# Performance work log

Hardware: AMD Instinct MI355X
Metric: run time of the kernel (lower is better)

## Reference

```python
import jax, jax.numpy as jnp
import numpy as np

N_EMBD = 1024
N_HEAD = 16
HEAD_DIM = N_EMBD // N_HEAD
EPS = 1e-8


def rmsnorm(x, scale):
    return x * jax.lax.rsqrt(jnp.mean(x * x, axis=-1, keepdims=True) + EPS) * scale


def setup_inputs() -> dict:
    key = jax.random.key(0)
    ks = jax.random.split(key, 7)
    B, L, D = 4, 2048, N_EMBD
    s = lambda fan_in: 1.0 / np.sqrt(fan_in)
    return {
        "x": jax.random.normal(ks[0], (B, L, D), jnp.float32),
        "norm1_scale": jnp.ones((D,), jnp.float32),
        "w_qkv": jax.random.normal(ks[1], (D, 3 * D), jnp.float32) * s(D),
        "w_proj": jax.random.normal(ks[2], (D, D), jnp.float32) * s(D),
        "norm2_scale": jnp.ones((D,), jnp.float32),
        "w_fc1": jax.random.normal(ks[3], (D, 4 * D), jnp.float32) * s(D),
        "w_fc2": jax.random.normal(ks[4], (4 * D, D), jnp.float32) * s(4 * D),
    }


def reference(x, norm1_scale, w_qkv, w_proj, norm2_scale, w_fc1, w_fc2):
    B, L, D = x.shape
    H, hd = N_HEAD, HEAD_DIM

    # --- attention sub-block ---
    h = rmsnorm(x, norm1_scale)
    qkv = h @ w_qkv  # [B, L, 3D]
    q, k, v = jnp.split(qkv, 3, axis=-1)
    q = q.reshape(B, L, H, hd).transpose(0, 2, 1, 3)  # [B, H, L, hd]
    k = k.reshape(B, L, H, hd).transpose(0, 2, 1, 3)
    v = v.reshape(B, L, H, hd).transpose(0, 2, 1, 3)
    att = jnp.einsum("bhqd,bhkd->bhqk", q, k) * (hd ** -0.5)
    att = jax.nn.softmax(att, axis=-1)  # bidirectional, no mask
    out = jnp.einsum("bhqk,bhkd->bhqd", att, v)
    out = out.transpose(0, 2, 1, 3).reshape(B, L, D)
    x = x + out @ w_proj

    # --- MLP sub-block ---
    h = rmsnorm(x, norm2_scale)
    x = x + jax.nn.gelu(h @ w_fc1, approximate=False) @ w_fc2
    return x
```

## Files before the change

kernel.cpp:

```cpp
#include <hip/hip_runtime.h>
#include <hip/hip_bf16.h>
#include <cmath>


typedef __bf16 bf16x8 __attribute__((ext_vector_type(8)));
typedef __bf16 bf16x2 __attribute__((ext_vector_type(2)));
typedef float f32x4 __attribute__((ext_vector_type(4)));

__device__ __forceinline__ float bf2f(unsigned short u) {
  union { unsigned int i; float f; } c; c.i = ((unsigned int)u) << 16; return c.f;
}
__device__ __forceinline__ unsigned short f2bf(float f) {
  union { unsigned int i; float f; } c; c.f = f;
  unsigned int r = c.i + 0x7fffu + ((c.i >> 16) & 1u);
  return (unsigned short)(r >> 16);
}

__device__ __forceinline__ bool probe_bf16(const void* p) {
  return *reinterpret_cast<const unsigned int*>(p) == 0x3F803F80u;
}
__device__ __forceinline__ float ldext(const void* p, size_t i, bool isbf) {
  return isbf ? bf2f(reinterpret_cast<const unsigned short*>(p)[i])
              : reinterpret_cast<const float*>(p)[i];
}

__device__ __forceinline__ void cp16(const unsigned short* g, unsigned short* l) {
  __builtin_amdgcn_global_load_lds(
      (const __attribute__((address_space(1))) unsigned int*)g,
      (__attribute__((address_space(3))) unsigned int*)l,
      16, 0, 0);
}

__global__ __launch_bounds__(256) void transpose_any(
    const void* __restrict__ in, unsigned short* __restrict__ out,
    int R, int C, const void* __restrict__ probe) {
  const bool isbf = probe_bf16(probe);
  __shared__ unsigned short tile[32][33];
  const int bx = blockIdx.x * 32;
  const int by = blockIdx.y * 32;
  const int tx = threadIdx.x & 31, ty = threadIdx.x >> 5;
#pragma unroll
  for (int i = 0; i < 32; i += 8)
    tile[ty + i][tx] = f2bf(ldext(in, (size_t)(by + ty + i) * C + bx + tx, isbf));
  __syncthreads();
#pragma unroll
  for (int i = 0; i < 32; i += 8)
    out[(size_t)(bx + ty + i) * R + by + tx] = tile[tx][ty + i];
}

__device__ __forceinline__ void rmsnorm_body(
    const float v0, const float v1, const float v2, const float v3,
    const void* scale, bool isbf, unsigned short* outrow, int tid) {
  float ss = v0 * v0 + v1 * v1 + v2 * v2 + v3 * v3;
#pragma unroll
  for (int m = 32; m >= 1; m >>= 1) ss += __shfl_xor(ss, m);
  __shared__ float red[4];
  if ((tid & 63) == 0) red[tid >> 6] = ss;
  __syncthreads();
  ss = red[0] + red[1] + red[2] + red[3];
  const float rstd = rsqrtf(ss * (1.0f / 1024.0f) + 1e-8f);
  ushort4 o;
  o.x = f2bf(v0 * rstd * ldext(scale, tid * 4 + 0, isbf));
  o.y = f2bf(v1 * rstd * ldext(scale, tid * 4 + 1, isbf));
  o.z = f2bf(v2 * rstd * ldext(scale, tid * 4 + 2, isbf));
  o.w = f2bf(v3 * rstd * ldext(scale, tid * 4 + 3, isbf));
  reinterpret_cast<ushort4*>(outrow)[tid] = o;
}

__global__ __launch_bounds__(256) void rmsnorm_ext(
    const void* __restrict__ x, const void* __restrict__ scale,
    unsigned short* __restrict__ out, const void* __restrict__ probe) {
  const bool isbf = probe_bf16(probe);
  const int row = blockIdx.x, tid = threadIdx.x;
  float v0, v1, v2, v3;
  if (isbf) {
    ushort4 u = reinterpret_cast<const ushort4*>(x)[(size_t)row * 256 + tid];
    v0 = bf2f(u.x); v1 = bf2f(u.y); v2 = bf2f(u.z); v3 = bf2f(u.w);
  } else {
    float4 f = reinterpret_cast<const float4*>(x)[(size_t)row * 256 + tid];
    v0 = f.x; v1 = f.y; v2 = f.z; v3 = f.w;
  }
  rmsnorm_body(v0, v1, v2, v3, scale, isbf, out + (size_t)row * 1024, tid);
}

__global__ __launch_bounds__(256) void rmsnorm_int(
    const unsigned short* __restrict__ x, const void* __restrict__ scale,
    unsigned short* __restrict__ out, const void* __restrict__ probe) {
  const bool isbf = probe_bf16(probe);
  const int row = blockIdx.x, tid = threadIdx.x;
  ushort4 u = reinterpret_cast<const ushort4*>(x + (size_t)row * 1024)[tid];
  rmsnorm_body(bf2f(u.x), bf2f(u.y), bf2f(u.z), bf2f(u.w),
               scale, isbf, out + (size_t)row * 1024, tid);
}

template <int EPI, typename OutT>
__global__ __launch_bounds__(256) void gemm_bt(
    const unsigned short* __restrict__ A, const unsigned short* __restrict__ BT,
    OutT* __restrict__ C, const void* __restrict__ Res,
    int M, int N, int K, const void* __restrict__ probe) {
  __shared__ __align__(16) unsigned short As[128 * 64];
  __shared__ __align__(16) unsigned short Bs[128 * 64];
  const int tid = threadIdx.x;
  const int lane = tid & 63;
  const int w = tid >> 6;
  const int quad = lane >> 4;
  const int l16 = lane & 15;
  const int wr = w >> 1, wc = w & 1;
  const int m0 = blockIdx.y * 128;
  const int n0 = blockIdx.x * 128;

  const f32x4 zero = {0.f, 0.f, 0.f, 0.f};
  f32x4 acc[4][4];
#pragma unroll
  for (int i = 0; i < 4; ++i)
#pragma unroll
    for (int j = 0; j < 4; ++j) acc[i][j] = zero;

  for (int kt = 0; kt < K; kt += 64) {
#pragma unroll
    for (int i = 0; i < 4; ++i) {
      const int cb = (i * 4 + w) * 64;
      const int c = cb + lane;
      const int row = c >> 3;
      const int gc = (c & 7) ^ (row & 7);
      cp16(A + (size_t)(m0 + row) * K + kt + gc * 8, As + (size_t)cb * 8);
      cp16(BT + (size_t)(n0 + row) * K + kt + gc * 8, Bs + (size_t)cb * 8);
    }
    __syncthreads();

#pragma unroll
    for (int kk = 0; kk < 2; ++kk) {
      bf16x8 af[4], bfr[4];
#pragma unroll
      for (int mi = 0; mi < 4; ++mi)
        af[mi] = *reinterpret_cast<const bf16x8*>(
            As + (wr * 64 + mi * 16 + l16) * 64 + ((((kk << 2) + quad) ^ (l16 & 7)) << 3));
#pragma unroll
      for (int ni = 0; ni < 4; ++ni)
        bfr[ni] = *reinterpret_cast<const bf16x8*>(
            Bs + (wc * 64 + ni * 16 + l16) * 64 + ((((kk << 2) + quad) ^ (l16 & 7)) << 3));
#pragma unroll
      for (int mi = 0; mi < 4; ++mi)
#pragma unroll
        for (int ni = 0; ni < 4; ++ni)
          acc[mi][ni] = __builtin_amdgcn_mfma_f32_16x16x32_bf16(af[mi], bfr[ni], acc[mi][ni], 0, 0, 0);
    }
    __syncthreads();
  }

  if constexpr (EPI == 5) {
    if (n0 >= 2048) {
      unsigned short* vt = (unsigned short*)Res;
#pragma unroll
      for (int mi = 0; mi < 4; ++mi) {
        const int r0 = m0 + wr * 64 + mi * 16 + quad * 4;
        const int bq = r0 >> 11;
        const int key = r0 & 2047;
#pragma unroll
        for (int ni = 0; ni < 4; ++ni) {
          const int vcol = n0 - 2048 + wc * 64 + ni * 16 + l16;
          ushort4 o4;
          o4.x = f2bf(acc[mi][ni][0]); o4.y = f2bf(acc[mi][ni][1]);
          o4.z = f2bf(acc[mi][ni][2]); o4.w = f2bf(acc[mi][ni][3]);
          *reinterpret_cast<ushort4*>(
              vt + (((size_t)(bq * 1024 + vcol)) << 11) + key) = o4;
        }
      }
      return;
    }
  }

  const bool pb = (EPI == 3) ? probe_bf16(probe) : true;
#pragma unroll
  for (int mi = 0; mi < 4; ++mi) {
#pragma unroll
    for (int reg = 0; reg < 4; ++reg) {
      const int row = m0 + wr * 64 + mi * 16 + quad * 4 + reg;
#pragma unroll
      for (int ni = 0; ni < 4; ++ni) {
        const int col = n0 + wc * 64 + ni * 16 + l16;
        float v = acc[mi][ni][reg];
        if (EPI == 1) v = 0.5f * v * (1.0f + erff(v * 0.70710678118654752f));
        if (EPI == 2) v += bf2f(reinterpret_cast<const unsigned short*>(Res)[(size_t)row * N + col]);
        if (EPI == 3) v += ldext(Res, (size_t)row * N + col, pb);
        if ((EPI == 4 || EPI == 5) && col < 1024) v *= 0.18033688011112042f;
        if constexpr (sizeof(OutT) == 2)
          C[(size_t)row * N + col] = f2bf(v);
        else
          C[(size_t)row * N + col] = v;
      }
    }
  }
}

__global__ __launch_bounds__(256) void flash_attn(
    const unsigned short* __restrict__ qkv,
    const unsigned short* __restrict__ vT,
    unsigned short* __restrict__ out) {
  __shared__ __align__(16) unsigned short Ks[2][64 * 64];
  __shared__ __align__(16) unsigned short Vs[2][64 * 64];
  const int L = 2048, DQ = 3072, D = 1024;
  const int qt = blockIdx.x, h = blockIdx.y, b = blockIdx.z;
  const int tid = threadIdx.x, lane = tid & 63, w = tid >> 6;
  const int quad = lane >> 4, l16 = lane & 15;
  const int woff = w * 32;
  const unsigned short* base = qkv + (size_t)b * L * DQ;
  const unsigned short* vbase = vT + (size_t)(b * 1024 + h * 64) * 2048;

  unsigned short* Qs = &Vs[0][0];
#pragma unroll
  for (int i = 0; i < 4; ++i) {
    const int cb = i * 256 + w * 64;
    const int c = cb + lane;
    const int r = c >> 3, d8 = (c & 7) << 3;
    cp16(base + (size_t)(qt * 128 + r) * DQ + h * 64 + d8, Qs + ((size_t)cb << 3));
  }
  asm volatile("s_waitcnt vmcnt(0)" ::: "memory");
  __builtin_amdgcn_s_barrier();
  __builtin_amdgcn_sched_barrier(0);
  bf16x8 qf[2][2];
#pragma unroll
  for (int mj = 0; mj < 2; ++mj)
#pragma unroll
    for (int kc = 0; kc < 2; ++kc)
      qf[mj][kc] = *reinterpret_cast<const bf16x8*>(
          Qs + (woff + mj * 16 + l16) * 64 + kc * 32 + quad * 8);
  asm volatile("s_waitcnt lgkmcnt(0)" ::: "memory");
  __builtin_amdgcn_sched_barrier(0);
  __builtin_amdgcn_s_barrier();

  auto STAGE = [&](int s, int kt0) {
#pragma unroll
    for (int i = 0; i < 2; ++i) {
      const int cb = i * 256 + w * 64;
      const int cd = cb + lane;
      const int m = cd >> 3, cc = cd & 7;
      const int gk = ((m >> 4) & 1) * 32 + ((m >> 2) & 3) * 8 + (m >> 5) * 4 + (m & 3);
      const int gc = cc ^ (m & 7);
      cp16(base + (size_t)(kt0 + gk) * DQ + 1024 + h * 64 + gc * 8,
           &Ks[s][(size_t)cb << 3]);
    }
#pragma unroll
    for (int i = 0; i < 2; ++i) {
      const int cb = i * 256 + w * 64;
      const int cd = cb + lane;
      const int d = cd >> 3, cc = cd & 7;
      const int gc = cc ^ (d & 7);
      cp16(vbase + (size_t)d * 2048 + kt0 + gc * 8, &Vs[s][(size_t)cb << 3]);
    }
  };

  STAGE(0, 0);

  const f32x4 zero = {0.f, 0.f, 0.f, 0.f};
  f32x4 l4[2] = {zero, zero};
  f32x4 o[2][4];
#pragma unroll
  for (int mj = 0; mj < 2; ++mj)
#pragma unroll
    for (int nd = 0; nd < 4; ++nd) o[mj][nd] = zero;

  for (int kt = 0; kt < L; kt += 64) {
    const int cur = (kt >> 6) & 1;
    if (kt + 64 < L) {
      STAGE(cur ^ 1, kt + 64);
      asm volatile("s_waitcnt vmcnt(4)" ::: "memory");
    } else {
      asm volatile("s_waitcnt vmcnt(0)" ::: "memory");
    }
    __builtin_amdgcn_s_barrier();
    __builtin_amdgcn_sched_barrier(0);

    f32x4 sv[4][2];
#pragma unroll
    for (int ki = 0; ki < 4; ++ki)
#pragma unroll
      for (int mj = 0; mj < 2; ++mj) sv[ki][mj] = zero;
#pragma unroll
    for (int kc = 0; kc < 2; ++kc) {
      bf16x8 kf[4];
#pragma unroll
      for (int ki = 0; ki < 4; ++ki)
        kf[ki] = *reinterpret_cast<const bf16x8*>(
            &Ks[cur][(ki * 16 + l16) * 64 + ((((kc << 2) + quad) ^ (l16 & 7)) << 3)]);
      __builtin_amdgcn_s_setprio(1);
#pragma unroll
      for (int ki = 0; ki < 4; ++ki)
#pragma unroll
        for (int mj = 0; mj < 2; ++mj)
          sv[ki][mj] = __builtin_amdgcn_mfma_f32_16x16x32_bf16(kf[ki], qf[mj][kc], sv[ki][mj], 0, 0, 0);
      __builtin_amdgcn_s_setprio(0);
    }

    bf16x8 pf[2][2];
#pragma unroll
    for (int mj = 0; mj < 2; ++mj)
#pragma unroll
      for (int kc = 0; kc < 2; ++kc) {
        f32x4 pa, pb;
#pragma unroll
        for (int r = 0; r < 4; ++r) pa[r] = __builtin_amdgcn_exp2f(sv[kc][mj][r]);
#pragma unroll
        for (int r = 0; r < 4; ++r) pb[r] = __builtin_amdgcn_exp2f(sv[kc + 2][mj][r]);
        l4[mj] += pa;
        l4[mj] += pb;
        bf16x8 t;
        t[0] = (__bf16)pa[0]; t[1] = (__bf16)pa[1]; t[2] = (__bf16)pa[2]; t[3] = (__bf16)pa[3];
        t[4] = (__bf16)pb[0]; t[5] = (__bf16)pb[1]; t[6] = (__bf16)pb[2]; t[7] = (__bf16)pb[3];
        pf[mj][kc] = t;
      }

#pragma unroll
    for (int kc = 0; kc < 2; ++kc) {
      bf16x8 vf[4];
#pragma unroll
      for (int nd = 0; nd < 4; ++nd)
        vf[nd] = *reinterpret_cast<const bf16x8*>(
            &Vs[cur][(nd * 16 + l16) * 64 + ((((kc << 2) + quad) ^ (l16 & 7)) << 3)]);
      __builtin_amdgcn_s_setprio(1);
#pragma unroll
      for (int mj = 0; mj < 2; ++mj)
#pragma unroll
        for (int nd = 0; nd < 4; ++nd)
          o[mj][nd] = __builtin_amdgcn_mfma_f32_16x16x32_bf16(pf[mj][kc], vf[nd], o[mj][nd], 0, 0, 0);
      __builtin_amdgcn_s_setprio(0);
    }

    if (kt + 64 < L) {
      asm volatile("s_waitcnt lgkmcnt(0)" ::: "memory");
      __builtin_amdgcn_sched_barrier(0);
      __builtin_amdgcn_s_barrier();
    }
  }

#pragma unroll
  for (int mj = 0; mj < 2; ++mj) {
    float lp = l4[mj][0] + l4[mj][1] + l4[mj][2] + l4[mj][3];
    lp += __shfl_xor(lp, 16);
    lp += __shfl_xor(lp, 32);
#pragma unroll
    for (int r = 0; r < 4; ++r) {
      const float inv = 1.0f / __shfl(lp, quad * 4 + r);
      const int row = qt * 128 + woff + mj * 16 + quad * 4 + r;
#pragma unroll
      for (int nd = 0; nd < 4; ++nd) {
        const int col = h * 64 + nd * 16 + l16;
        out[(size_t)(b * L + row) * D + col] = f2bf(o[mj][nd][r] * inv);
      }
    }
  }
}

extern "C" void kernel_launch(void* const* d_in, const int* in_sizes, int n_in,
                              void* d_out, int out_size, void* d_ws, size_t ws_size,
                              hipStream_t stream) {
  const void* x      = d_in[0];
  const void* n1s    = d_in[1];
  const void* w_qkv  = d_in[2];
  const void* w_proj = d_in[3];
  const void* n2s    = d_in[4];
  const void* w_fc1  = d_in[5];
  const void* w_fc2  = d_in[6];
  float* out = (float*)d_out;
  char* ws = (char*)d_ws;

  const int M = 8192;
  unsigned short* wqkvT  = (unsigned short*)(ws + ((size_t)0   << 20));
  unsigned short* wprojT = (unsigned short*)(ws + ((size_t)6   << 20));
  unsigned short* wfc1T  = (unsigned short*)(ws + ((size_t)8   << 20));
  unsigned short* wfc2T  = (unsigned short*)(ws + ((size_t)16  << 20));
  unsigned short* h      = (unsigned short*)(ws + ((size_t)24  << 20));
  unsigned short* qkvb   = (unsigned short*)(ws + ((size_t)40  << 20));
  unsigned short* attn   = (unsigned short*)(ws + ((size_t)88  << 20));
  unsigned short* x2     = (unsigned short*)(ws + ((size_t)104 << 20));
  unsigned short* g      = qkvb;
  unsigned short* vT     = x2;

  transpose_any<<<dim3(96, 32), 256, 0, stream>>>(w_qkv, wqkvT, 1024, 3072, n1s);
  transpose_any<<<dim3(32, 32), 256, 0, stream>>>(w_proj, wprojT, 1024, 1024, n1s);
  transpose_any<<<dim3(128, 32), 256, 0, stream>>>(w_fc1, wfc1T, 1024, 4096, n1s);
  transpose_any<<<dim3(32, 128), 256, 0, stream>>>(w_fc2, wfc2T, 4096, 1024, n1s);

  rmsnorm_ext<<<M, 256, 0, stream>>>(x, n1s, h, n1s);
  gemm_bt<5, unsigned short><<<dim3(24, 64), 256, 0, stream>>>(h, wqkvT, qkvb, vT, M, 3072, 1024, n1s);
  flash_attn<<<dim3(16, 16, 4), 256, 0, stream>>>(qkvb, vT, attn);
  gemm_bt<3, unsigned short><<<dim3(8, 64), 256, 0, stream>>>(attn, wprojT, x2, x, M, 1024, 1024, n1s);
  rmsnorm_int<<<M, 256, 0, stream>>>(x2, n2s, h, n1s);
  gemm_bt<1, unsigned short><<<dim3(32, 64), 256, 0, stream>>>(h, wfc1T, g, nullptr, M, 4096, 1024, n1s);
  gemm_bt<2, float><<<dim3(8, 64), 256, 0, stream>>>(g, wfc2T, out, x2, M, 1024, 4096, n1s);
}
```

Measured before the change: 568.9 us.

## Add 256x256 eight-wave ping-pong pipelined GEMM for QKV and FC1

Introduces a new GEMM kernel using 256x256 output tiles, 512 threads, double-buffered LDS split into halves, and explicit phase scheduling with barriers, setprio and waitcnt. This interleaves async global-to-LDS copies with MFMA sub-phases. QKV and FC1 projections now use it, with the QKV scaling and V-transpose epilogue moved into the new kernel. The aim is higher MFMA utilisation and more operand reuse per loaded tile. The trade-offs are much higher register pressure, 128KB of LDS per block, and fewer blocks, which may leave CUs underfilled.

```diff
diff --git a/kernel.cpp b/kernel.cpp
--- a/kernel.cpp
+++ b/kernel.cpp
@@ -91,6 +91,158 @@
   ushort4 u = reinterpret_cast<const ushort4*>(x + (size_t)row * 1024)[tid];
   rmsnorm_body(bf2f(u.x), bf2f(u.y), bf2f(u.z), bf2f(u.w),
                scale, isbf, out + (size_t)row * 1024, tid);
+}
+
+#define PH_PRE { __builtin_amdgcn_s_barrier(); \
+  asm volatile("s_waitcnt lgkmcnt(0)" ::: "memory"); \
+  __builtin_amdgcn_sched_barrier(0); \
+  __builtin_amdgcn_s_setprio(1); }
+#define PH_POST { __builtin_amdgcn_s_setprio(0); __builtin_amdgcn_s_barrier(); }
+
+#define LDA_(par, mh) \
+  _Pragma("unroll") for (int mi = 0; mi < 4; ++mi) \
+  _Pragma("unroll") for (int kk = 0; kk < 2; ++kk) \
+    afr[mi][kk] = *reinterpret_cast<const bf16x8*>( \
+        &As[par][mh][(wr * 64 + mi * 16 + l16) * 64 + ((((kk << 2) + quad) ^ (l16 & 7)) << 3)]);
+
+#define LDB_(par, nh, dst) \
+  _Pragma("unroll") for (int ni = 0; ni < 2; ++ni) \
+  _Pragma("unroll") for (int kk = 0; kk < 2; ++kk) \
+    dst[ni][kk] = *reinterpret_cast<const bf16x8*>( \
+        &Bs[par][nh][(wc * 32 + ni * 16 + l16) * 64 + ((((kk << 2) + quad) ^ (l16 & 7)) << 3)]);
+
+#define MM_(bfx, mh, nh) \
+  _Pragma("unroll") for (int kk = 0; kk < 2; ++kk) \
+  _Pragma("unroll") for (int mi = 0; mi < 4; ++mi) \
+  _Pragma("unroll") for (int ni = 0; ni < 2; ++ni) \
+    acc[(mh) * 4 + mi][(nh) * 2 + ni] = __builtin_amdgcn_mfma_f32_16x16x32_bf16( \
+        afr[mi][kk], bfx[ni][kk], acc[(mh) * 4 + mi][(nh) * 2 + ni], 0, 0, 0);
+
+#define SA_(par, hh, kt) { \
+  cp16(A + oA[0][hh] + (kt), &As[par][hh][(w * 64) * 8]); \
+  cp16(A + oA[1][hh] + (kt), &As[par][hh][(512 + w * 64) * 8]); }
+#define SB_(par, hh, kt) { \
+  cp16(BT + oB[0][hh] + (kt), &Bs[par][hh][(w * 64) * 8]); \
+  cp16(BT + oB[1][hh] + (kt), &Bs[par][hh][(512 + w * 64) * 8]); }
+
+#define TILE_(par, tt) { \
+  const int kt1 = ((tt) + 1) << 6; \
+  const int kt2 = ((tt) + 2) << 6; \
+  LDA_(par, 0); LDB_(par, 0, bf0); \
+  if (kt1 < K) SA_(par ^ 1, 1, kt1); \
+  PH_PRE; MM_(bf0, 0, 0); PH_POST; \
+  LDB_(par, 1, bf1); \
+  if (kt2 < K) SA_(par, 0, kt2); \
+  PH_PRE; MM_(bf1, 0, 1); PH_POST; \
+  LDA_(par, 1); \
+  if (kt2 < K) SB_(par, 0, kt2); \
+  PH_PRE; MM_(bf1, 1, 1); PH_POST; \
+  if (kt2 < K) SB_(par, 1, kt2); \
+  PH_PRE; MM_(bf0, 1, 0); \
+  __builtin_amdgcn_s_setprio(0); \
+  if (kt2 < K)      { asm volatile("s_waitcnt vmcnt(6)" ::: "memory"); } \
+  else if (kt1 < K) { asm volatile("s_waitcnt vmcnt(0)" ::: "memory"); } \
+  if (kt1 < K) __builtin_amdgcn_s_barrier(); }
+
+template <int EPI, typename OutT>
+__global__ __launch_bounds__(512, 2) void gemm8p(
+    const unsigned short* __restrict__ A, const unsigned short* __restrict__ BT,
+    OutT* __restrict__ C, const void* __restrict__ Res,
+    int M, int N, int K, const void* __restrict__ probe) {
+  __shared__ __align__(16) unsigned short As[2][2][128 * 64];
+  __shared__ __align__(16) unsigned short Bs[2][2][128 * 64];
+  const int tid = threadIdx.x;
+  const int lane = tid & 63;
+  const int w = tid >> 6;
+  const int quad = lane >> 4, l16 = lane & 15;
+  const int wr = w >> 2, wc = w & 3;
+  const int m0 = blockIdx.y * 256;
+  const int n0 = blockIdx.x * 256;
+  const int nt = K >> 6;
+
+  size_t oA[2][2], oB[2][2];
+#pragma unroll
+  for (int i = 0; i < 2; ++i) {
+    const int c = i * 512 + w * 64 + lane;
+    const int r = c >> 3;
+    const int gc = (c & 7) ^ (r & 7);
+#pragma unroll
+    for (int hh = 0; hh < 2; ++hh) {
+      oA[i][hh] = (size_t)(m0 + hh * 128 + r) * K + gc * 8;
+      oB[i][hh] = (size_t)(n0 + hh * 128 + r) * K + gc * 8;
+    }
+  }
+
+  const f32x4 zero = {0.f, 0.f, 0.f, 0.f};
+  f32x4 acc[8][4];
+#pragma unroll
+  for (int i = 0; i < 8; ++i)
+#pragma unroll
+    for (int j = 0; j < 4; ++j) acc[i][j] = zero;
+
+  SA_(0, 0, 0); SB_(0, 0, 0); SB_(0, 1, 0); SA_(0, 1, 0);
+  if (K > 64) {
+    SA_(1, 0, 64); SB_(1, 0, 64); SB_(1, 1, 64);
+    asm volatile("s_waitcnt vmcnt(6)" ::: "memory");
+  } else {
+    asm volatile("s_waitcnt vmcnt(0)" ::: "memory");
+  }
+  __builtin_amdgcn_s_barrier();
+
+  bf16x8 afr[4][2], bf0[2][2], bf1[2][2];
+  for (int t = 0; t < nt; t += 2) {
+    TILE_(0, t);
+    TILE_(1, t + 1);
+  }
+
+  if constexpr (EPI == 5) {
+    if (n0 >= 2048) {
+      unsigned short* vt = (unsigned short*)Res;
+#pragma unroll
+      for (int mh = 0; mh < 2; ++mh)
+#pragma unroll
+        for (int mi = 0; mi < 4; ++mi) {
+          const int r0 = m0 + mh * 128 + wr * 64 + mi * 16 + quad * 4;
+          const int bq = r0 >> 11;
+          const int key = r0 & 2047;
+#pragma unroll
+          for (int nh = 0; nh < 2; ++nh)
+#pragma unroll
+            for (int ni = 0; ni < 2; ++ni) {
+              const int vcol = n0 - 2048 + nh * 128 + wc * 32 + ni * 16 + l16;
+              const f32x4 a4 = acc[mh * 4 + mi][nh * 2 + ni];
+              ushort4 o4;
+              o4.x = f2bf(a4[0]); o4.y = f2bf(a4[1]);
+              o4.z = f2bf(a4[2]); o4.w = f2bf(a4[3]);
+              *reinterpret_cast<ushort4*>(
+                  vt + (((size_t)(bq * 1024 + vcol)) << 11) + key) = o4;
+            }
+        }
+      return;
+    }
+  }
+
+#pragma unroll
+  for (int mh = 0; mh < 2; ++mh)
+#pragma unroll
+    for (int mi = 0; mi < 4; ++mi)
+#pragma unroll
+      for (int reg = 0; reg < 4; ++reg) {
+        const int row = m0 + mh * 128 + wr * 64 + mi * 16 + quad * 4 + reg;
+#pragma unroll
+        for (int nh = 0; nh < 2; ++nh)
+#pragma unroll
+          for (int ni = 0; ni < 2; ++ni) {
+            const int col = n0 + nh * 128 + wc * 32 + ni * 16 + l16;
+            float v = acc[mh * 4 + mi][nh * 2 + ni][reg];
+            if (EPI == 1) v = 0.5f * v * (1.0f + erff(v * 0.70710678118654752f));
+            if (EPI == 5 && col < 1024) v *= 0.18033688011112042f;
+            if constexpr (sizeof(OutT) == 2)
+              C[(size_t)row * N + col] = f2bf(v);
+            else
+              C[(size_t)row * N + col] = v;
+          }
+      }
 }
 
 template <int EPI, typename OutT>
@@ -148,28 +300,6 @@
     __syncthreads();
   }
 
-  if constexpr (EPI == 5) {
-    if (n0 >= 2048) {
-      unsigned short* vt = (unsigned short*)Res;
-#pragma unroll
-      for (int mi = 0; mi < 4; ++mi) {
-        const int r0 = m0 + wr * 64 + mi * 16 + quad * 4;
-        const int bq = r0 >> 11;
-        const int key = r0 & 2047;
-#pragma unroll
-        for (int ni = 0; ni < 4; ++ni) {
-          const int vcol = n0 - 2048 + wc * 64 + ni * 16 + l16;
-          ushort4 o4;
-          o4.x = f2bf(acc[mi][ni][0]); o4.y = f2bf(acc[mi][ni][1]);
-          o4.z = f2bf(acc[mi][ni][2]); o4.w = f2bf(acc[mi][ni][3]);
-          *reinterpret_cast<ushort4*>(
-              vt + (((size_t)(bq * 1024 + vcol)) << 11) + key) = o4;
-        }
-      }
-      return;
-    }
-  }
-
   const bool pb = (EPI == 3) ? probe_bf16(probe) : true;
 #pragma unroll
   for (int mi = 0; mi < 4; ++mi) {
@@ -183,7 +313,6 @@
         if (EPI == 1) v = 0.5f * v * (1.0f + erff(v * 0.70710678118654752f));
         if (EPI == 2) v += bf2f(reinterpret_cast<const unsigned short*>(Res)[(size_t)row * N + col]);
         if (EPI == 3) v += ldext(Res, (size_t)row * N + col, pb);
-        if ((EPI == 4 || EPI == 5) && col < 1024) v *= 0.18033688011112042f;
         if constexpr (sizeof(OutT) == 2)
           C[(size_t)row * N + col] = f2bf(v);
         else
@@ -382,10 +511,10 @@
   transpose_any<<<dim3(32, 128), 256, 0, stream>>>(w_fc2, wfc2T, 4096, 1024, n1s);
 
   rmsnorm_ext<<<M, 256, 0, stream>>>(x, n1s, h, n1s);
-  gemm_bt<5, unsigned short><<<dim3(24, 64), 256, 0, stream>>>(h, wqkvT, qkvb, vT, M, 3072, 1024, n1s);
+  gemm8p<5, unsigned short><<<dim3(12, 32), 512, 0, stream>>>(h, wqkvT, qkvb, vT, M, 3072, 1024, n1s);
   flash_attn<<<dim3(16, 16, 4), 256, 0, stream>>>(qkvb, vT, attn);
   gemm_bt<3, unsigned short><<<dim3(8, 64), 256, 0, stream>>>(attn, wprojT, x2, x, M, 1024, 1024, n1s);
   rmsnorm_int<<<M, 256, 0, stream>>>(x2, n2s, h, n1s);
-  gemm_bt<1, unsigned short><<<dim3(32, 64), 256, 0, stream>>>(h, wfc1T, g, nullptr, M, 4096, 1024, n1s);
+  gemm8p<1, unsigned short><<<dim3(16, 32), 512, 0, stream>>>(h, wfc1T, g, nullptr, M, 4096, 1024, n1s);
   gemm_bt<2, float><<<dim3(8, 64), 256, 0, stream>>>(g, wfc2T, out, x2, M, 1024, 4096, n1s);
 }
```

Result: no change. 561.1 us (-1.4%).
